# Optimization experiments

Measured on AMD Instinct MI355X. Metric: run time of the kernel, lower is better.

## Reference

```python
import jax, jax.numpy as jnp
import numpy as np

# Config mirrors init_kwargs
B, C, K, D = 32768, 100, 8, 512
ROUTING_T = 0.07      # routing_temperature
PRIOR_T = 0.07        # class_prior_temperature
SUB_T = 0.05          # subproto_temperature
RIDGE = 0.1           # ridge (fixed mode)
EPS = 1e-8            # input_norm_eps
PROTO_INIT_SCALE = 0.02


def _l2norm(x, eps=EPS):
    # F.normalize(p=2, dim=-1, eps=eps)
    n = jnp.linalg.norm(x, axis=-1, keepdims=True)
    return x / jnp.maximum(n, eps)


def setup_inputs() -> dict:
    key = jax.random.key(0)
    k1, k2 = jax.random.split(key)
    h = jax.random.normal(k1, (B, D), dtype=jnp.float32)
    # learned parameter: prototypes [num_classes, protos_per_class, feature_dim]
    prototypes = jax.random.normal(k2, (C, K, D), dtype=jnp.float32) * PROTO_INIT_SCALE
    return {"h": h, "prototypes": prototypes}


def reference(h, prototypes):
    # ---- input normalization (input_norm_mode='l2_hypersphere') ----
    hn = _l2norm(h)                                   # [B, D]
    Pn = _l2norm(prototypes)                          # [C, K, D]

    # ---- prototype-distance routing (cosine sims, multiple temperatures) ----
    cos = jnp.einsum('bd,ckd->bck', hn, Pn)           # [B, C, K]
    w_sub = jax.nn.softmax(cos / SUB_T, axis=-1)      # subproto routing weights
    class_sim = jnp.sum(w_sub * cos, axis=-1)         # pooled aggregation [B, C]
    prior_logits = class_sim / PRIOR_T                # class prior logits

    # ---- per-class closed-form ridge solve (same_opp_balanced support) ----
    # Support for class c: its K sub-prototypes (target +1, total weight 0.5)
    # vs. the other C-1 class centers (target -1, total weight 0.5).
    centers = _l2norm(jnp.mean(Pn, axis=1))           # [C, D] pooled class centers
    ws = 0.5 / K
    wo = 0.5 / (C - 1)

    # Gram of same-class support, batched over classes: [C, D, D]
    G_same = ws * jnp.einsum('ckd,cke->cde', Pn, Pn)
    # Opp gram = all-centers gram minus own center outer product
    S_all = centers.T @ centers                       # [D, D]
    G_opp = wo * (S_all[None, :, :] - jnp.einsum('cd,ce->cde', centers, centers))
    A = G_same + G_opp + RIDGE * jnp.eye(D, dtype=h.dtype)  # [C, D, D]

    # RHS X^T S y: +1 on same protos, -1 on opp centers
    b_same = ws * jnp.sum(Pn, axis=1)                 # [C, D]
    csum = jnp.sum(centers, axis=0)                   # [D]
    b_opp = -wo * (csum[None, :] - centers)           # [C, D]
    b = b_same + b_opp

    W = jnp.linalg.solve(A, b[..., None])[..., 0]     # [C, D] per-class ridge weights

    # ---- residual head: routed closed-form logits added to prior ----
    residual = (hn @ W.T) / ROUTING_T                 # [B, C]
    return prior_logits + residual
```

## Files before the change

kernel.cpp:

```cpp
#include <hip/hip_runtime.h>
#include <math.h>

#define NB 32768
#define NC 100
#define NK 8
#define ND 512
#define ALPHA 22.0f
#define NEU_ITERS 12

typedef __attribute__((ext_vector_type(8))) short short8;
typedef __attribute__((ext_vector_type(4))) float f32x4;

__device__ __forceinline__ void gl_lds16(const void* g, void* l) {
    __builtin_amdgcn_global_load_lds(
        (const __attribute__((address_space(1))) void*)g,
        (__attribute__((address_space(3))) void*)l, 16, 0, 0);
}

__device__ __forceinline__ float warpReduceSum(float v) {
#pragma unroll
    for (int off = 32; off > 0; off >>= 1) v += __shfl_xor(v, off);
    return v;
}

__device__ float blockReduceSum256(float v, float* red) {
    int tid = threadIdx.x;
    v = warpReduceSum(v);
    __syncthreads();
    if ((tid & 63) == 0) red[tid >> 6] = v;
    __syncthreads();
    return red[0] + red[1] + red[2] + red[3];
}

__device__ __forceinline__ unsigned short f2bf(float x) {
    unsigned u = __float_as_uint(x);
    u = (u + 0x7FFFu + ((u >> 16) & 1u)) >> 16;
    return (unsigned short)u;
}
__device__ __forceinline__ float bf2f(unsigned short h) {
    return __uint_as_float(((unsigned)h) << 16);
}


__global__ void k_prep_class(const float* __restrict__ protos, float* __restrict__ X,
                             float* __restrict__ centersT, unsigned short* __restrict__ Bp) {
    __shared__ float red[4];
    int c = blockIdx.x;
    int tid = threadIdx.x;
    const float eps = 1e-8f;
    float pv0[NK], pv1[NK];
#pragma unroll
    for (int k = 0; k < NK; ++k) {
        pv0[k] = protos[(c * NK + k) * ND + tid];
        pv1[k] = protos[(c * NK + k) * ND + tid + 256];
    }
    float sv0 = 0.f, sv1 = 0.f;
#pragma unroll
    for (int k = 0; k < NK; ++k) {
        float ss = blockReduceSum256(pv0[k] * pv0[k] + pv1[k] * pv1[k], red);
        float inv = 1.0f / fmaxf(sqrtf(ss), eps);
        pv0[k] *= inv; pv1[k] *= inv;
        X[(c * NK + k) * ND + tid] = pv0[k];
        X[(c * NK + k) * ND + tid + 256] = pv1[k];
        Bp[(size_t)(c * 10 + k) * ND + tid] = f2bf(pv0[k]);
        Bp[(size_t)(c * 10 + k) * ND + tid + 256] = f2bf(pv1[k]);
        sv0 += pv0[k]; sv1 += pv1[k];
    }
    float ssum = blockReduceSum256(sv0 * sv0 + sv1 * sv1, red);
    float mnorm = sqrtf(ssum) * 0.125f;
    float cinv = 0.125f / fmaxf(mnorm, eps);
    float* centers = X + 800 * ND;
    float c0 = sv0 * cinv, c1 = sv1 * cinv;
    centers[c * ND + tid] = c0;
    centers[c * ND + tid + 256] = c1;
    centersT[tid * NC + c] = c0;
    centersT[(tid + 256) * NC + c] = c1;
    const float ws = 0.5f / 8.0f;
    float* bvec = X + 900 * ND;
    bvec[c * ND + tid] = ws * sv0;
    bvec[c * ND + tid + 256] = ws * sv1;
}

__global__ void k_csbopp(float* __restrict__ X) {
    int c = blockIdx.x, tid = threadIdx.x;
    const float wo = 0.5f / 99.0f;
    const float* centers = X + 800 * ND;
    float* bvec = X + 900 * ND;
#pragma unroll
    for (int h = 0; h < 2; ++h) {
        int d = tid + h * 256;
        float s = 0.f;
#pragma unroll 4
        for (int i = 0; i < NC; ++i) s += centers[i * ND + d];
        bvec[c * ND + d] -= wo * (s - centers[c * ND + d]);
    }
}

__global__ __launch_bounds__(256) void k_T1M(const float* __restrict__ X,
                                             const float* __restrict__ centersT,
                                             float* __restrict__ T1, float* __restrict__ M) {
    __shared__ float xs[4][ND];
    int tid = threadIdx.x;
    int wave = tid >> 6, lane = tid & 63;
    int j = blockIdx.x * 4 + wave;
    reinterpret_cast<float4*>(xs[wave])[lane * 2] =
        reinterpret_cast<const float4*>(X + (size_t)j * ND)[lane * 2];
    reinterpret_cast<float4*>(xs[wave])[lane * 2 + 1] =
        reinterpret_cast<const float4*>(X + (size_t)j * ND)[lane * 2 + 1];
    __syncthreads();
    int i0 = lane, i1 = lane + 64;
    int i1c = (i1 < NC) ? i1 : 0;
    float s0 = 0.f, s1 = 0.f;
#pragma unroll 8
    for (int d = 0; d < ND; ++d) {
        float xv = xs[wave][d];
        s0 = fmaf(xv, centersT[d * NC + i0], s0);
        s1 = fmaf(xv, centersT[d * NC + i1c], s1);
    }
    T1[j * NC + i0] = s0;
    if (i1 < NC) T1[j * NC + i1] = s1;
    if (j >= 800 && j < 900) {
        int ci = j - 800;
        float a0 = s0 + ((i0 == ci) ? 19.8f : 0.f);
        M[ci * NC + i0] = ((i0 == ci) ? 1.f : 0.f) - a0 * (1.0f / ALPHA);
        if (i1 < NC) {
            float a1 = s1 + ((i1 == ci) ? 19.8f : 0.f);
            M[ci * NC + i1] = ((i1 == ci) ? 1.f : 0.f) - a1 * (1.0f / ALPHA);
        }
    }
}

__global__ __launch_bounds__(256) void k_T2neu(const float* __restrict__ M,
                                               const float* __restrict__ T1,
                                               float* __restrict__ T2) {
    __shared__ float Msh[NC * 108];
    __shared__ float pbuf[2][4][104];
    int tid = threadIdx.x;
    int wave = tid >> 6, lane = tid & 63;
    int j = blockIdx.x * 4 + wave;
    for (int idx = tid; idx < NC * NC; idx += 256) {
        int i = idx / NC, m = idx - i * NC;
        Msh[i * 108 + m] = M[idx];
    }
    int i0 = lane;
    int i1 = lane + 64;
    int i1c = (i1 < NC) ? i1 : 0;
    float t0 = T1[j * NC + i0];
    float t1v = (i1 < NC) ? T1[j * NC + i1] : 0.f;
    float s0 = t0, s1 = t1v;
    pbuf[0][wave][i0] = t0;
    if (i1 < NC) pbuf[0][wave][i1] = t1v;
    __syncthreads();
    int cur = 0;
    for (int it = 0; it < NEU_ITERS; ++it) {
        const float* p = pbuf[cur][wave];
        float y0 = 0.f, y1 = 0.f;
#pragma unroll 5
        for (int m = 0; m < NC; m += 4) {
            float4 pv = *reinterpret_cast<const float4*>(p + m);
            float4 a0 = *reinterpret_cast<const float4*>(&Msh[i0 * 108 + m]);
            float4 a1 = *reinterpret_cast<const float4*>(&Msh[i1c * 108 + m]);
            y0 = fmaf(a0.x, pv.x, y0); y0 = fmaf(a0.y, pv.y, y0);
            y0 = fmaf(a0.z, pv.z, y0); y0 = fmaf(a0.w, pv.w, y0);
            y1 = fmaf(a1.x, pv.x, y1); y1 = fmaf(a1.y, pv.y, y1);
            y1 = fmaf(a1.z, pv.z, y1); y1 = fmaf(a1.w, pv.w, y1);
        }
        s0 += y0; s1 += y1;
        int nxt = cur ^ 1;
        pbuf[nxt][wave][i0] = y0;
        if (i1 < NC) pbuf[nxt][wave][i1] = y1;
        cur = nxt;
    }
    T2[j * NC + i0] = s0 * (1.0f / ALPHA);
    if (i1 < NC) T2[j * NC + i1] = s1 * (1.0f / ALPHA);
}

__global__ __launch_bounds__(256) void k_solveW(const float* __restrict__ X,
                                                const float* __restrict__ T1,
                                                const float* __restrict__ T2,
                                                unsigned short* __restrict__ Bp) {
    int c = blockIdx.x, tid = threadIdx.x;
    if (c >= NC) {
        uint4 z = {0, 0, 0, 0};
        for (int idx = tid; idx < 10 * ND / 8; idx += 256)
            reinterpret_cast<uint4*>(Bp + (size_t)c * 10 * ND)[idx] = z;
        return;
    }
    __shared__ float Xs[10 * 516];
    __shared__ float T1s[10 * 104];
    __shared__ float T2s[10 * 104];
    __shared__ float G[10][10];
    __shared__ float SL[9 * 10];
    __shared__ float zL[9];
    __shared__ float q[104];
    for (int idx = tid; idx < 10 * 128; idx += 256) {
        int a = idx >> 7, p = idx & 127;
        int row = (a < 8) ? (c * 8 + a) : ((a == 8) ? (800 + c) : (900 + c));
        reinterpret_cast<float4*>(&Xs[a * 516])[p] =
            reinterpret_cast<const float4*>(X + (size_t)row * ND)[p];
    }
    for (int idx = tid; idx < 10 * NC; idx += 256) {
        int a = idx / NC, i = idx - a * NC;
        int row = (a < 8) ? (c * 8 + a) : ((a == 8) ? (800 + c) : (900 + c));
        T1s[a * 104 + i] = T1[row * NC + i];
        T2s[a * 104 + i] = T2[row * NC + i];
    }
    __syncthreads();
    if (tid < 100) {
        int a = tid / 10, b = tid - (tid / 10) * 10;
        float s = 0.f;
        for (int d = 0; d < ND; ++d) s += Xs[a * 516 + d] * Xs[b * 516 + d];
        G[a][b] = s;
    }
    __syncthreads();
    if (tid < 90) {
        int a = tid / 10, b = tid - (tid / 10) * 10;
        float s = 0.f;
#pragma unroll 4
        for (int i = 0; i < NC; ++i) s += T1s[a * 104 + i] * T2s[b * 104 + i];
        float val = (G[a][b] - s) * 10.0f;
        if (b == a) val += (a < 8) ? 16.0f : -198.0f;
        SL[tid] = val;
    }
    __syncthreads();
    if (tid == 0) {
        for (int p = 0; p < 9; ++p) {
            int best = p; float bv = fabsf(SL[p * 10 + p]);
            for (int r = p + 1; r < 9; ++r) {
                float v = fabsf(SL[r * 10 + p]);
                if (v > bv) { bv = v; best = r; }
            }
            if (best != p)
                for (int j = p; j < 10; ++j) {
                    float t = SL[p * 10 + j]; SL[p * 10 + j] = SL[best * 10 + j]; SL[best * 10 + j] = t;
                }
            float ip = 1.0f / SL[p * 10 + p];
            for (int r = p + 1; r < 9; ++r) {
                float f = SL[r * 10 + p] * ip;
                for (int j = p; j < 10; ++j) SL[r * 10 + j] -= f * SL[p * 10 + j];
            }
        }
        for (int p = 8; p >= 0; --p) {
            float s = SL[p * 10 + 9];
            for (int j = p + 1; j < 9; ++j) s -= SL[p * 10 + j] * zL[j];
            zL[p] = s / SL[p * 10 + p];
        }
    }
    __syncthreads();
    if (tid < NC) {
        float s = T2s[9 * 104 + tid];
#pragma unroll
        for (int a = 0; a < 9; ++a) s -= zL[a] * T2s[a * 104 + tid];
        q[tid] = s;
    }
    __syncthreads();
    const float* centers = X + 800 * ND;
#pragma unroll
    for (int h = 0; h < 2; ++h) {
        int d = tid + h * 256;
        float u = Xs[9 * 516 + d];
#pragma unroll
        for (int a = 0; a < 9; ++a) u -= zL[a] * Xs[a * 516 + d];
        float s = 0.f;
#pragma unroll 4
        for (int i = 0; i < NC; ++i) s = fmaf(centers[i * ND + d], q[i], s);
        float w = (u - s) * 10.0f;
        unsigned short hi = f2bf(w);
        Bp[(size_t)(c * 10 + 8) * ND + d] = hi;
        Bp[(size_t)(c * 10 + 9) * ND + d] = f2bf(w - bf2f(hi));
    }
}


__global__ void k_hn(const float* __restrict__ h, unsigned short* __restrict__ hnb) {
    int tid = threadIdx.x;
    int wave = tid >> 6, lane = tid & 63;
    int r = blockIdx.x * 4 + wave;
    const float4* hp = reinterpret_cast<const float4*>(h + (size_t)r * ND);
    float4 v0 = hp[lane * 2];
    float4 v1 = hp[lane * 2 + 1];
    float s = v0.x * v0.x + v0.y * v0.y + v0.z * v0.z + v0.w * v0.w
            + v1.x * v1.x + v1.y * v1.y + v1.z * v1.z + v1.w * v1.w;
    s = warpReduceSum(s);
    float inv = 1.0f / fmaxf(sqrtf(s), 1e-8f);
    uint4 o;
    o.x = (unsigned)f2bf(v0.x * inv) | ((unsigned)f2bf(v0.y * inv) << 16);
    o.y = (unsigned)f2bf(v0.z * inv) | ((unsigned)f2bf(v0.w * inv) << 16);
    o.z = (unsigned)f2bf(v1.x * inv) | ((unsigned)f2bf(v1.y * inv) << 16);
    o.w = (unsigned)f2bf(v1.z * inv) | ((unsigned)f2bf(v1.w * inv) << 16);
    reinterpret_cast<uint4*>(hnb + (size_t)r * ND)[lane] = o;
}


__global__ __launch_bounds__(256, 2) void k_main_mfma(
        const unsigned short* __restrict__ hnb, const unsigned short* __restrict__ Bp,
        float* __restrict__ out) {
    __shared__ __align__(16) char smem[57344];
    float* Cs = (float*)smem;

    int tid = threadIdx.x;
    int wave = tid >> 6, lane = tid & 63;
    int m = lane & 15, g = lane >> 4;
    int rs = m & 7;
    int rh = wave & 1, ch = wave >> 1;

    int id = blockIdx.x;
    int xcd = id & 7, kk2 = id >> 3;
    int cb = kk2 % 7;
    int rb = (kk2 / 7) * 8 + xcd;
    int r0 = rb * 64;

    int rsub = lane >> 3;
    int osw = (lane & 7) ^ rsub;

    f32x4 acc[2][5] = {};

    auto issue = [&](int kc, int p) {
        unsigned short* As = (unsigned short*)(smem + p * 28672);
        unsigned short* Bs = As + 4096;
#pragma unroll
        for (int q2 = 0; q2 < 2; ++q2) {
            int chk = wave * 2 + q2;
            gl_lds16(hnb + (size_t)(r0 + chk * 8 + rsub) * ND + kc * 64 + osw * 8,
                     As + chk * 512);
        }
#pragma unroll
        for (int q2 = 0; q2 < 5; ++q2) {
            int chk = wave * 5 + q2;
            gl_lds16(Bp + (size_t)(cb * 160 + chk * 8 + rsub) * ND + kc * 64 + osw * 8,
                     Bs + chk * 512);
        }
    };

    issue(0, 0);
    for (int kc = 0; kc < 8; ++kc) {
        int cur = kc & 1;
        __syncthreads();
        if (kc < 7) issue(kc + 1, cur ^ 1);
        unsigned short* As = (unsigned short*)(smem + cur * 28672);
        unsigned short* Bs = As + 4096;
#pragma unroll
        for (int kk = 0; kk < 2; ++kk) {
            short8 af[2], bfr[5];
#pragma unroll
            for (int rt = 0; rt < 2; ++rt)
                af[rt] = *reinterpret_cast<const short8*>(
                    As + (rh * 32 + rt * 16 + m) * 64 + (((kk << 2) + g) ^ rs) * 8);
#pragma unroll
            for (int ct = 0; ct < 5; ++ct)
                bfr[ct] = *reinterpret_cast<const short8*>(
                    Bs + (ch * 80 + ct * 16 + m) * 64 + (((kk << 2) + g) ^ rs) * 8);
#pragma unroll
            for (int rt = 0; rt < 2; ++rt)
#pragma unroll
                for (int ct = 0; ct < 5; ++ct)
                    acc[rt][ct] = __builtin_amdgcn_mfma_f32_16x16x32_bf16(
                        af[rt], bfr[ct], acc[rt][ct], 0, 0, 0);
        }
    }

    __syncthreads();
#pragma unroll
    for (int rt = 0; rt < 2; ++rt)
#pragma unroll
        for (int ct = 0; ct < 5; ++ct)
#pragma unroll
            for (int reg = 0; reg < 4; ++reg) {
                int lr = rh * 32 + rt * 16 + g * 4 + reg;
                int lc = ch * 80 + ct * 16 + m;
                Cs[lr * 163 + lc] = acc[rt][ct][reg];
            }
    __syncthreads();
    {
        int cl = tid & 15;
        int c = cb * 16 + cl;
#pragma unroll
        for (int q2 = 0; q2 < 4; ++q2) {
            int r = (tid >> 4) + q2 * 16;
            float v[10];
#pragma unroll
            for (int j = 0; j < 10; ++j) v[j] = Cs[r * 163 + cl * 10 + j];
            float mx = v[0];
#pragma unroll
            for (int j = 1; j < 8; ++j) mx = fmaxf(mx, v[j]);
            float se = 0.f, sec = 0.f;
#pragma unroll
            for (int j = 0; j < 8; ++j) {
                float e = __expf((v[j] - mx) * 20.0f);
                se += e; sec += e * v[j];
            }
            float res = v[8] + v[9];
            if (c < NC)
                out[(size_t)(r0 + r) * NC + c] = (sec / se + res) * (1.0f / 0.07f);
        }
    }
}

extern "C" void kernel_launch(void* const* d_in, const int* in_sizes, int n_in,
                              void* d_out, int out_size, void* d_ws, size_t ws_size,
                              hipStream_t stream) {
    (void)in_sizes; (void)n_in; (void)out_size; (void)ws_size;
    const float* h = (const float*)d_in[0];
    const float* protos = (const float*)d_in[1];
    float* out = (float*)d_out;
    float* ws = (float*)d_ws;

    float* X        = ws;
    float* centersT = X + 512000;
    float* M        = centersT + 51200;
    float* T1       = M + 10000;
    float* T2       = T1 + 100000;
    unsigned short* hnb = (unsigned short*)(T2 + 100000);
    unsigned short* Bp  = hnb + (size_t)NB * ND;

    k_hn<<<NB / 4, 256, 0, stream>>>(h, hnb);
    k_prep_class<<<NC, 256, 0, stream>>>(protos, X, centersT, Bp);
    k_csbopp<<<NC, 256, 0, stream>>>(X);
    k_T1M<<<250, 256, 0, stream>>>(X, centersT, T1, M);
    k_T2neu<<<250, 256, 0, stream>>>(M, T1, T2);
    k_solveW<<<112, 256, 0, stream>>>(X, T1, T2, Bp);
    k_main_mfma<<<3584, 256, 0, stream>>>(hnb, Bp, out);
}
```

Before: 241.3 us.

## Rewrite main GEMM with 32x32 MFMA, direct register loads and larger row tiles

The main kernel drops LDS staging via global_load_lds and double buffering. Each wave now loads bf16 fragments straight from global memory into registers with a two-stage software prefetch and uses 32x32x16 MFMA instructions. Each block now covers 256 rows instead of 64, cutting the grid from 3584 to 896 blocks, and the epilogue runs in four passes through a smaller LDS tile. The softmax max-subtraction is removed, which relies on cosines being bounded so exp(20*v) cannot overflow. The workspace layout is also reordered to put the bf16 buffers first.

```diff
diff --git a/kernel.cpp b/kernel.cpp
--- a/kernel.cpp
+++ b/kernel.cpp
@@ -10,12 +10,7 @@
 
 typedef __attribute__((ext_vector_type(8))) short short8;
 typedef __attribute__((ext_vector_type(4))) float f32x4;
-
-__device__ __forceinline__ void gl_lds16(const void* g, void* l) {
-    __builtin_amdgcn_global_load_lds(
-        (const __attribute__((address_space(1))) void*)g,
-        (__attribute__((address_space(3))) void*)l, 16, 0, 0);
-}
+typedef __attribute__((ext_vector_type(16))) float f32x16;
 
 __device__ __forceinline__ float warpReduceSum(float v) {
 #pragma unroll
@@ -295,103 +290,91 @@
 __global__ __launch_bounds__(256, 2) void k_main_mfma(
         const unsigned short* __restrict__ hnb, const unsigned short* __restrict__ Bp,
         float* __restrict__ out) {
-    __shared__ __align__(16) char smem[57344];
-    float* Cs = (float*)smem;
-
+    __shared__ float Cs[64 * 161];
     int tid = threadIdx.x;
     int wave = tid >> 6, lane = tid & 63;
-    int m = lane & 15, g = lane >> 4;
-    int rs = m & 7;
-    int rh = wave & 1, ch = wave >> 1;
+    int lo = lane & 31, hi = lane >> 5;
 
     int id = blockIdx.x;
-    int xcd = id & 7, kk2 = id >> 3;
-    int cb = kk2 % 7;
-    int rb = (kk2 / 7) * 8 + xcd;
-    int r0 = rb * 64;
-
-    int rsub = lane >> 3;
-    int osw = (lane & 7) ^ rsub;
-
-    f32x4 acc[2][5] = {};
-
-    auto issue = [&](int kc, int p) {
-        unsigned short* As = (unsigned short*)(smem + p * 28672);
-        unsigned short* Bs = As + 4096;
-#pragma unroll
-        for (int q2 = 0; q2 < 2; ++q2) {
-            int chk = wave * 2 + q2;
-            gl_lds16(hnb + (size_t)(r0 + chk * 8 + rsub) * ND + kc * 64 + osw * 8,
-                     As + chk * 512);
-        }
-#pragma unroll
-        for (int q2 = 0; q2 < 5; ++q2) {
-            int chk = wave * 5 + q2;
-            gl_lds16(Bp + (size_t)(cb * 160 + chk * 8 + rsub) * ND + kc * 64 + osw * 8,
-                     Bs + chk * 512);
-        }
-    };
-
-    issue(0, 0);
-    for (int kc = 0; kc < 8; ++kc) {
-        int cur = kc & 1;
+    int xcd = id & 7, t = id >> 3;
+    int cb = t >> 4;
+    int rr = t & 15;
+    int r0 = (rr * 8 + xcd) * 256;
+
+    const unsigned short* pa0 = hnb + (size_t)(r0 + wave * 32 + lo) * ND + hi * 8;
+    const unsigned short* pa1 = pa0 + 128 * ND;
+    const unsigned short* pb0 = Bp + (size_t)(cb * 160 + lo) * ND + hi * 8;
+
+    f32x16 acc[2][5] = {};
+    short8 a0[2], b0[5], a1[2], b1[5];
+
+    a0[0] = *(const short8*)pa0;
+    a0[1] = *(const short8*)pa1;
+#pragma unroll
+    for (int ct = 0; ct < 5; ++ct)
+        b0[ct] = *(const short8*)(pb0 + (size_t)ct * 32 * ND);
+    pa0 += 16; pa1 += 16; pb0 += 16;
+
+#pragma unroll 1
+    for (int ks = 0; ks < 32; ks += 2) {
+        a1[0] = *(const short8*)pa0;
+        a1[1] = *(const short8*)pa1;
+#pragma unroll
+        for (int ct = 0; ct < 5; ++ct)
+            b1[ct] = *(const short8*)(pb0 + (size_t)ct * 32 * ND);
+#pragma unroll
+        for (int rt = 0; rt < 2; ++rt)
+#pragma unroll
+            for (int ct = 0; ct < 5; ++ct)
+                acc[rt][ct] = __builtin_amdgcn_mfma_f32_32x32x16_bf16(
+                    a0[rt], b0[ct], acc[rt][ct], 0, 0, 0);
+        a0[0] = *(const short8*)(pa0 + 16);
+        a0[1] = *(const short8*)(pa1 + 16);
+#pragma unroll
+        for (int ct = 0; ct < 5; ++ct)
+            b0[ct] = *(const short8*)(pb0 + (size_t)ct * 32 * ND + 16);
+#pragma unroll
+        for (int rt = 0; rt < 2; ++rt)
+#pragma unroll
+            for (int ct = 0; ct < 5; ++ct)
+                acc[rt][ct] = __builtin_amdgcn_mfma_f32_32x32x16_bf16(
+                    a1[rt], b1[ct], acc[rt][ct], 0, 0, 0);
+        pa0 += 32; pa1 += 32; pb0 += 32;
+    }
+
+#pragma unroll 1
+    for (int p = 0; p < 4; ++p) {
         __syncthreads();
-        if (kc < 7) issue(kc + 1, cur ^ 1);
-        unsigned short* As = (unsigned short*)(smem + cur * 28672);
-        unsigned short* Bs = As + 4096;
-#pragma unroll
-        for (int kk = 0; kk < 2; ++kk) {
-            short8 af[2], bfr[5];
-#pragma unroll
-            for (int rt = 0; rt < 2; ++rt)
-                af[rt] = *reinterpret_cast<const short8*>(
-                    As + (rh * 32 + rt * 16 + m) * 64 + (((kk << 2) + g) ^ rs) * 8);
+        if ((wave >> 1) == (p & 1)) {
+            int rt = p >> 1;
+            int lrb = (wave & 1) * 32;
 #pragma unroll
             for (int ct = 0; ct < 5; ++ct)
-                bfr[ct] = *reinterpret_cast<const short8*>(
-                    Bs + (ch * 80 + ct * 16 + m) * 64 + (((kk << 2) + g) ^ rs) * 8);
-#pragma unroll
-            for (int rt = 0; rt < 2; ++rt)
-#pragma unroll
-                for (int ct = 0; ct < 5; ++ct)
-                    acc[rt][ct] = __builtin_amdgcn_mfma_f32_16x16x32_bf16(
-                        af[rt], bfr[ct], acc[rt][ct], 0, 0, 0);
-        }
-    }
-
-    __syncthreads();
-#pragma unroll
-    for (int rt = 0; rt < 2; ++rt)
-#pragma unroll
-        for (int ct = 0; ct < 5; ++ct)
-#pragma unroll
-            for (int reg = 0; reg < 4; ++reg) {
-                int lr = rh * 32 + rt * 16 + g * 4 + reg;
-                int lc = ch * 80 + ct * 16 + m;
-                Cs[lr * 163 + lc] = acc[rt][ct][reg];
-            }
-    __syncthreads();
-    {
+#pragma unroll
+                for (int reg = 0; reg < 16; ++reg) {
+                    int lr = lrb + (reg & 3) + 8 * (reg >> 2) + 4 * hi;
+                    Cs[lr * 161 + ct * 32 + lo] = acc[rt][ct][reg];
+                }
+        }
+        __syncthreads();
         int cl = tid & 15;
         int c = cb * 16 + cl;
-#pragma unroll
-        for (int q2 = 0; q2 < 4; ++q2) {
-            int r = (tid >> 4) + q2 * 16;
-            float v[10];
-#pragma unroll
-            for (int j = 0; j < 10; ++j) v[j] = Cs[r * 163 + cl * 10 + j];
-            float mx = v[0];
-#pragma unroll
-            for (int j = 1; j < 8; ++j) mx = fmaxf(mx, v[j]);
-            float se = 0.f, sec = 0.f;
-#pragma unroll
-            for (int j = 0; j < 8; ++j) {
-                float e = __expf((v[j] - mx) * 20.0f);
-                se += e; sec += e * v[j];
+        if (c < NC) {
+#pragma unroll
+            for (int q = 0; q < 4; ++q) {
+                int r = (tid >> 4) + q * 16;
+                float v[10];
+#pragma unroll
+                for (int j = 0; j < 10; ++j) v[j] = Cs[r * 161 + cl * 10 + j];
+                float se = 0.f, sec = 0.f;
+#pragma unroll
+                for (int j = 0; j < 8; ++j) {
+                    float e = __expf(v[j] * 20.0f);
+                    se += e; sec += e * v[j];
+                }
+                out[(size_t)(r0 + p * 64 + r) * NC + c] =
+                    (sec / se + (v[8] + v[9])) * (1.0f / 0.07f);
             }
-            float res = v[8] + v[9];
-            if (c < NC)
-                out[(size_t)(r0 + r) * NC + c] = (sec / se + res) * (1.0f / 0.07f);
         }
     }
 }
@@ -403,15 +386,14 @@
     const float* h = (const float*)d_in[0];
     const float* protos = (const float*)d_in[1];
     float* out = (float*)d_out;
-    float* ws = (float*)d_ws;
-
-    float* X        = ws;
+
+    unsigned short* hnb = (unsigned short*)d_ws;
+    unsigned short* Bp  = hnb + (size_t)NB * ND;
+    float* X        = (float*)(Bp + 1120 * ND);
     float* centersT = X + 512000;
     float* M        = centersT + 51200;
     float* T1       = M + 10000;
     float* T2       = T1 + 100000;
-    unsigned short* hnb = (unsigned short*)(T2 + 100000);
-    unsigned short* Bp  = hnb + (size_t)NB * ND;
 
     k_hn<<<NB / 4, 256, 0, stream>>>(h, hnb);
     k_prep_class<<<NC, 256, 0, stream>>>(protos, X, centersT, Bp);
@@ -419,5 +401,5 @@
     k_T1M<<<250, 256, 0, stream>>>(X, centersT, T1, M);
     k_T2neu<<<250, 256, 0, stream>>>(M, T1, T2);
     k_solveW<<<112, 256, 0, stream>>>(X, T1, T2, Bp);
-    k_main_mfma<<<3584, 256, 0, stream>>>(hnb, Bp, out);
-}
+    k_main_mfma<<<896, 256, 0, stream>>>(hnb, Bp, out);
+}
```

Result: slower. 335.0 us (+38.8%).

## Enlarge GEMM row tile to 128, drop LDS double buffering, raise occupancy

Applied to the files above, without the earlier changes.

The main MFMA kernel now computes 128 rows per block instead of 64, so each B tile loaded into LDS is reused across twice as many rows and the grid is halved. The double-buffered prefetch is replaced by a single buffer with load-then-sync per k-chunk. The smaller LDS footprint allows launch bounds of 4 blocks per CU, relying on occupancy to hide load latency. The epilogue is done in four 32-row passes through LDS, and the workspace is reordered so the bf16 buffers come first. The risks are exposed load latency without prefetch, more accumulator registers per thread, and extra barriers in the epilogue.

```diff
diff --git a/kernel.cpp b/kernel.cpp
--- a/kernel.cpp
+++ b/kernel.cpp
@@ -292,66 +292,59 @@
 }
 
 
-__global__ __launch_bounds__(256, 2) void k_main_mfma(
+__global__ __launch_bounds__(256, 4) void k_main_mfma(
         const unsigned short* __restrict__ hnb, const unsigned short* __restrict__ Bp,
         float* __restrict__ out) {
-    __shared__ __align__(16) char smem[57344];
+    __shared__ __align__(16) char smem[36864];
+    unsigned short* As = (unsigned short*)smem;
+    unsigned short* Bs = (unsigned short*)smem + 8192;
     float* Cs = (float*)smem;
 
     int tid = threadIdx.x;
     int wave = tid >> 6, lane = tid & 63;
     int m = lane & 15, g = lane >> 4;
     int rs = m & 7;
-    int rh = wave & 1, ch = wave >> 1;
+    int rowhalf = wave & 1, colhalf = wave >> 1;
 
     int id = blockIdx.x;
-    int xcd = id & 7, kk2 = id >> 3;
-    int cb = kk2 % 7;
-    int rb = (kk2 / 7) * 8 + xcd;
-    int r0 = rb * 64;
+    int xcd = id & 7, t = id >> 3;
+    int cb = t % 7;
+    int rr = t / 7;
+    int r0 = (rr * 8 + xcd) * 128;
 
     int rsub = lane >> 3;
     int osw = (lane & 7) ^ rsub;
 
-    f32x4 acc[2][5] = {};
-
-    auto issue = [&](int kc, int p) {
-        unsigned short* As = (unsigned short*)(smem + p * 28672);
-        unsigned short* Bs = As + 4096;
-#pragma unroll
-        for (int q2 = 0; q2 < 2; ++q2) {
-            int chk = wave * 2 + q2;
-            gl_lds16(hnb + (size_t)(r0 + chk * 8 + rsub) * ND + kc * 64 + osw * 8,
-                     As + chk * 512);
-        }
-#pragma unroll
-        for (int q2 = 0; q2 < 5; ++q2) {
-            int chk = wave * 5 + q2;
-            gl_lds16(Bp + (size_t)(cb * 160 + chk * 8 + rsub) * ND + kc * 64 + osw * 8,
-                     Bs + chk * 512);
-        }
-    };
-
-    issue(0, 0);
+    f32x4 acc[4][5] = {};
+
     for (int kc = 0; kc < 8; ++kc) {
-        int cur = kc & 1;
         __syncthreads();
-        if (kc < 7) issue(kc + 1, cur ^ 1);
-        unsigned short* As = (unsigned short*)(smem + cur * 28672);
-        unsigned short* Bs = As + 4096;
+#pragma unroll
+        for (int q = 0; q < 4; ++q) {
+            int ch = wave * 4 + q;
+            gl_lds16(hnb + (size_t)(r0 + ch * 8 + rsub) * ND + kc * 64 + osw * 8,
+                     As + ch * 512);
+        }
+#pragma unroll
+        for (int q = 0; q < 5; ++q) {
+            int ch = wave * 5 + q;
+            gl_lds16(Bp + (size_t)(cb * 160 + ch * 8 + rsub) * ND + kc * 64 + osw * 8,
+                     Bs + ch * 512);
+        }
+        __syncthreads();
 #pragma unroll
         for (int kk = 0; kk < 2; ++kk) {
-            short8 af[2], bfr[5];
-#pragma unroll
-            for (int rt = 0; rt < 2; ++rt)
+            short8 af[4], bfr[5];
+#pragma unroll
+            for (int rt = 0; rt < 4; ++rt)
                 af[rt] = *reinterpret_cast<const short8*>(
-                    As + (rh * 32 + rt * 16 + m) * 64 + (((kk << 2) + g) ^ rs) * 8);
+                    As + (rowhalf * 64 + rt * 16 + m) * 64 + (((kk << 2) + g) ^ rs) * 8);
 #pragma unroll
             for (int ct = 0; ct < 5; ++ct)
                 bfr[ct] = *reinterpret_cast<const short8*>(
-                    Bs + (ch * 80 + ct * 16 + m) * 64 + (((kk << 2) + g) ^ rs) * 8);
-#pragma unroll
-            for (int rt = 0; rt < 2; ++rt)
+                    Bs + (colhalf * 80 + ct * 16 + m) * 64 + (((kk << 2) + g) ^ rs) * 8);
+#pragma unroll
+            for (int rt = 0; rt < 4; ++rt)
 #pragma unroll
                 for (int ct = 0; ct < 5; ++ct)
                     acc[rt][ct] = __builtin_amdgcn_mfma_f32_16x16x32_bf16(
@@ -359,39 +352,47 @@
         }
     }
 
-    __syncthreads();
-#pragma unroll
-    for (int rt = 0; rt < 2; ++rt)
-#pragma unroll
-        for (int ct = 0; ct < 5; ++ct)
-#pragma unroll
-            for (int reg = 0; reg < 4; ++reg) {
-                int lr = rh * 32 + rt * 16 + g * 4 + reg;
-                int lc = ch * 80 + ct * 16 + m;
-                Cs[lr * 163 + lc] = acc[rt][ct][reg];
+#pragma unroll 1
+    for (int p = 0; p < 4; ++p) {
+        __syncthreads();
+        if (rowhalf == (p >> 1)) {
+#pragma unroll
+            for (int rt2 = 0; rt2 < 2; ++rt2) {
+                int rt = ((p & 1) << 1) + rt2;
+#pragma unroll
+                for (int ct = 0; ct < 5; ++ct)
+#pragma unroll
+                    for (int reg = 0; reg < 4; ++reg) {
+                        int lr = rt2 * 16 + g * 4 + reg;
+                        int lc = colhalf * 80 + ct * 16 + m;
+                        Cs[lr * 163 + lc] = acc[rt][ct][reg];
+                    }
             }
-    __syncthreads();
-    {
-        int cl = tid & 15;
-        int c = cb * 16 + cl;
-#pragma unroll
-        for (int q2 = 0; q2 < 4; ++q2) {
-            int r = (tid >> 4) + q2 * 16;
-            float v[10];
-#pragma unroll
-            for (int j = 0; j < 10; ++j) v[j] = Cs[r * 163 + cl * 10 + j];
-            float mx = v[0];
-#pragma unroll
-            for (int j = 1; j < 8; ++j) mx = fmaxf(mx, v[j]);
-            float se = 0.f, sec = 0.f;
-#pragma unroll
-            for (int j = 0; j < 8; ++j) {
-                float e = __expf((v[j] - mx) * 20.0f);
-                se += e; sec += e * v[j];
+        }
+        __syncthreads();
+        {
+            int cl = tid & 15;
+            int c = cb * 16 + cl;
+            if (c < NC) {
+#pragma unroll
+                for (int q = 0; q < 2; ++q) {
+                    int r = (tid >> 4) + q * 16;
+                    float v[10];
+#pragma unroll
+                    for (int j = 0; j < 10; ++j) v[j] = Cs[r * 163 + cl * 10 + j];
+                    float mx = v[0];
+#pragma unroll
+                    for (int j = 1; j < 8; ++j) mx = fmaxf(mx, v[j]);
+                    float se = 0.f, sec = 0.f;
+#pragma unroll
+                    for (int j = 0; j < 8; ++j) {
+                        float e = __expf((v[j] - mx) * 20.0f);
+                        se += e; sec += e * v[j];
+                    }
+                    out[(size_t)(r0 + p * 32 + r) * NC + c] =
+                        (sec / se + (v[8] + v[9])) * (1.0f / 0.07f);
+                }
             }
-            float res = v[8] + v[9];
-            if (c < NC)
-                out[(size_t)(r0 + r) * NC + c] = (sec / se + res) * (1.0f / 0.07f);
         }
     }
 }
@@ -403,15 +404,14 @@
     const float* h = (const float*)d_in[0];
     const float* protos = (const float*)d_in[1];
     float* out = (float*)d_out;
-    float* ws = (float*)d_ws;
-
-    float* X        = ws;
+
+    unsigned short* hnb = (unsigned short*)d_ws;
+    unsigned short* Bp  = hnb + (size_t)NB * ND;
+    float* X        = (float*)(Bp + 1120 * ND);
     float* centersT = X + 512000;
     float* M        = centersT + 51200;
     float* T1       = M + 10000;
     float* T2       = T1 + 100000;
-    unsigned short* hnb = (unsigned short*)(T2 + 100000);
-    unsigned short* Bp  = hnb + (size_t)NB * ND;
 
     k_hn<<<NB / 4, 256, 0, stream>>>(h, hnb);
     k_prep_class<<<NC, 256, 0, stream>>>(protos, X, centersT, Bp);
@@ -419,5 +419,5 @@
     k_T1M<<<250, 256, 0, stream>>>(X, centersT, T1, M);
     k_T2neu<<<250, 256, 0, stream>>>(M, T1, T2);
     k_solveW<<<112, 256, 0, stream>>>(X, T1, T2, Bp);
-    k_main_mfma<<<3584, 256, 0, stream>>>(hnb, Bp, out);
-}
+    k_main_mfma<<<1792, 256, 0, stream>>>(hnb, Bp, out);
+}
```

New measurement: 677.7 us. 2.81x slower.
